# Performance work log

Hardware: AMD Instinct MI355X
Metric: run time of the kernel (lower is better)

The kernel has to match this reference:

```python
import jax, jax.numpy as jnp
import numpy as np

DIM = 256
HEADS = 4
HEAD_DIM = 32
HIDDEN = HEADS * HEAD_DIM  # 128
EPS = 1e-12  # F.normalize eps


def rmsnorm(x, g):
    # F.normalize(x, dim=1) * g * sqrt(C)
    n = jnp.sqrt(jnp.sum(x * x, axis=1, keepdims=True))
    return x / jnp.maximum(n, EPS) * g * jnp.sqrt(jnp.float32(x.shape[1]))


def setup_inputs() -> dict:
    key = jax.random.key(0)
    k1, k2, k3 = jax.random.split(key, 3)
    b, h, w = 16, 64, 64
    x = jax.random.normal(k1, (b, DIM, h, w), dtype=jnp.float32)
    # conv weights: kaiming-ish scale for 1x1 convs
    w_qkv = jax.random.normal(k2, (3 * HIDDEN, DIM), dtype=jnp.float32) / np.sqrt(DIM)
    w_out = jax.random.normal(k3, (DIM, HIDDEN), dtype=jnp.float32) / np.sqrt(HIDDEN)
    return {
        "x": x,
        "g_norm": jnp.ones((1, DIM, 1, 1), jnp.float32),
        "w_qkv": w_qkv,
        "w_out": w_out,
        "b_out": jnp.zeros((DIM,), jnp.float32),
        "g_out": jnp.ones((1, DIM, 1, 1), jnp.float32),
    }


def reference(x, g_norm, w_qkv, w_out, b_out, g_out):
    b, c, h, w = x.shape
    n = h * w
    scale = HEAD_DIM ** (-0.5)

    xn = rmsnorm(x, g_norm)
    # 1x1 conv == channel matmul: (3*hidden, c) x (b, c, h, w)
    qkv = jnp.einsum('oc,bchw->bohw', w_qkv, xn)
    qkv = qkv.reshape(b, 3, HEADS, HEAD_DIM, n)
    q, k, v = qkv[:, 0], qkv[:, 1], qkv[:, 2]  # each (b, heads, head_dim, n)

    q = jax.nn.softmax(q, axis=-2)  # over head_dim
    k = jax.nn.softmax(k, axis=-1)  # over spatial tokens

    # context = k @ v^T : (b, heads, d, d)
    context = jnp.einsum('bhdn,bhen->bhde', k, v)
    # out = context^T @ (q*scale) : (b, heads, d, n)
    out = jnp.einsum('bhde,bhdn->bhen', context, q * scale)
    out = out.reshape(b, HIDDEN, h, w)

    out = jnp.einsum('oc,bchw->bohw', w_out, out) + b_out[None, :, None, None]
    out = rmsnorm(out, g_out)
    return out
```

## Files before the change

### kernel.cpp

```cpp
#include <hip/hip_runtime.h>
#include <hip/hip_bf16.h>
#include <math.h>

#define B 16
#define C 256
#define H 4
#define D 32
#define HID 128
#define O3 384
#define N 4096
#define NSPLIT 32
#define QSCALE 0.17677669529663687f
#define RMS_MUL 16.0f
#define EPS 1e-12f

typedef __attribute__((ext_vector_type(8))) short short8;
typedef __attribute__((ext_vector_type(4))) float f32x4;

__device__ __forceinline__ ushort f2bf(float f) {
  __hip_bfloat16 h = __float2bfloat16(f);
  return *(ushort*)&h;
}
__device__ __forceinline__ float bf2f(ushort u) {
  unsigned int v = ((unsigned int)u) << 16;
  return *(float*)&v;
}
__device__ __forceinline__ void load_lds16(const void* g, void* l) {
  __builtin_amdgcn_global_load_lds((const __attribute__((address_space(1))) void*)g,
                                   (__attribute__((address_space(3))) void*)l, 16, 0, 0);
}

__global__ __launch_bounds__(256) void k_prep(const float* __restrict__ wqkv,
                                              const float* __restrict__ g,
                                              const float* __restrict__ x,
                                              ushort* __restrict__ wA,
                                              ushort* __restrict__ xbf) {
  __shared__ float red[8][32];
  __shared__ float invs[32];
  int t = threadIdx.x;
  if (blockIdx.x < 384) {
    int idx = blockIdx.x * 256 + t;
    wA[idx] = f2bf(wqkv[idx] * g[idx & (C - 1)]);
    return;
  }
  int id = blockIdx.x - 384;
  int g8 = t >> 5, ln = t & 31;
  int b = id >> 7, n0 = (id & 127) * 32;
  const float* xb = x + (size_t)b * C * N + n0 + ln;
  float v[32];
  float ss = 0.f;
  #pragma unroll
  for (int i = 0; i < 32; ++i) {
    v[i] = xb[(size_t)(g8 * 32 + i) * N];
    ss += v[i] * v[i];
  }
  red[g8][ln] = ss;
  __syncthreads();
  if (t < 32) {
    float tot = 0.f;
    #pragma unroll
    for (int j = 0; j < 8; ++j) tot += red[j][t];
    invs[t] = RMS_MUL / fmaxf(sqrtf(tot), EPS);
  }
  __syncthreads();
  float inv = invs[ln];
  ushort* dst = xbf + ((size_t)(b * N + n0 + ln)) * C + g8 * 32;
  #pragma unroll
  for (int ch = 0; ch < 4; ++ch) {
    union { ushort s[8]; uint4 q; } u;
    #pragma unroll
    for (int j = 0; j < 8; ++j) u.s[j] = f2bf(v[ch * 8 + j] * inv);
    *(uint4*)(dst + ch * 8) = u.q;
  }
}

__global__ __launch_bounds__(256, 4) void k_kvctx(const ushort* __restrict__ A,
                                                  const ushort* __restrict__ Bm,
                                                  float* __restrict__ ctxp) {
  const int K = 256;
  __shared__ ushort lds[16384];
  ushort* Abuf = lds;
  ushort* Bbuf = lds + 8192;
  int bid = blockIdx.x;
  int work = (bid & 7) * 128 + (bid >> 3);
  int mh = work & 1, sl = (work >> 1) & 31, b = work >> 6;
  int t = threadIdx.x;
  int lane = t & 63, w = t >> 6;
  int n0 = sl * 128;
  const ushort* Bb = Bm + ((size_t)b * N + n0) * K;
  f32x4 acc[2][8] = {};
  for (int k0 = 0; k0 < K; k0 += 64) {
    #pragma unroll
    for (int i = 0; i < 4; ++i) {
      int c = w * 4 + i;
      int lr = c * 8 + (lane >> 3);
      int gr = mh * 64 + (lr & 63) + ((lr & 64) << 1);
      int col = k0 + (lane & 7) * 8;
      load_lds16(A + (size_t)gr * K + col, Abuf + c * 512);
    }
    #pragma unroll
    for (int i = 0; i < 4; ++i) {
      int c = w * 4 + i;
      int row = c * 8 + (lane >> 3);
      int col = k0 + (lane & 7) * 8;
      load_lds16(Bb + (size_t)row * K + col, Bbuf + c * 512);
    }
    __syncthreads();
    #pragma unroll
    for (int kk = 0; kk < 2; ++kk) {
      short8 af[2], bfr[8];
      #pragma unroll
      for (int m = 0; m < 2; ++m)
        af[m] = *(const short8*)&Abuf[(w * 32 + m * 16 + (lane & 15)) * 64 + kk * 32 + (lane >> 4) * 8];
      #pragma unroll
      for (int nn = 0; nn < 8; ++nn)
        bfr[nn] = *(const short8*)&Bbuf[(nn * 16 + (lane & 15)) * 64 + kk * 32 + (lane >> 4) * 8];
      #pragma unroll
      for (int m = 0; m < 2; ++m)
        #pragma unroll
        for (int nn = 0; nn < 8; ++nn)
          acc[m][nn] = __builtin_amdgcn_mfma_f32_16x16x32_bf16(af[m], bfr[nn], acc[m][nn], 0, 0, 0);
    }
    __syncthreads();
  }
  float* cbb = ctxp + (size_t)(sl * 64 + b * 4) * 1056;
  if (w < 2) {
    #pragma unroll
    for (int m = 0; m < 2; ++m)
      #pragma unroll
      for (int nn = 0; nn < 8; ++nn)
        #pragma unroll
        for (int j = 0; j < 4; ++j) acc[m][nn][j] = __expf(acc[m][nn][j]);
    #pragma unroll
    for (int m = 0; m < 2; ++m)
      #pragma unroll
      for (int j = 0; j < 4; ++j) {
        float s = 0.f;
        #pragma unroll
        for (int nn = 0; nn < 8; ++nn) s += acc[m][nn][j];
        s += __shfl_xor(s, 1); s += __shfl_xor(s, 2);
        s += __shfl_xor(s, 4); s += __shfl_xor(s, 8);
        if ((lane & 15) == 0) {
          int lr = w * 32 + m * 16 + (lane >> 4) * 4 + j;
          int h = mh * 2 + (lr >> 5);
          cbb[(size_t)h * 1056 + 1024 + (lr & 31)] = s;
        }
      }
  }
  #pragma unroll
  for (int m = 0; m < 2; ++m)
    #pragma unroll
    for (int nn = 0; nn < 8; ++nn) {
      int lr0 = w * 32 + m * 16 + (lane >> 4) * 4;
      int n = nn * 16 + (lane & 15);
      #pragma unroll
      for (int j = 0; j < 4; ++j) {
        int lr = lr0 + j;
        lds[(lr * 128 + n) ^ ((lr & 7) << 3)] = f2bf(acc[m][nn][j]);
      }
    }
  __syncthreads();
  int hl = w >> 1, eh = w & 1;
  f32x4 cacc[2] = {};
  #pragma unroll
  for (int kk = 0; kk < 4; ++kk) {
    short8 af2[2], bv;
    #pragma unroll
    for (int m = 0; m < 2; ++m) {
      int lrk = hl * 32 + m * 16 + (lane & 15);
      af2[m] = *(const short8*)&lds[(lrk * 128 + kk * 32 + (lane >> 4) * 8) ^ ((lrk & 7) << 3)];
    }
    int lrv = 64 + hl * 32 + eh * 16 + (lane & 15);
    bv = *(const short8*)&lds[(lrv * 128 + kk * 32 + (lane >> 4) * 8) ^ ((lrv & 7) << 3)];
    #pragma unroll
    for (int m = 0; m < 2; ++m)
      cacc[m] = __builtin_amdgcn_mfma_f32_16x16x32_bf16(af2[m], bv, cacc[m], 0, 0, 0);
  }
  int hg = mh * 2 + hl;
  float* cb = ctxp + (size_t)(sl * 64 + b * 4 + hg) * 1056;
  #pragma unroll
  for (int m = 0; m < 2; ++m)
    #pragma unroll
    for (int j = 0; j < 4; ++j) {
      int d = m * 16 + (lane >> 4) * 4 + j;
      int e = eh * 16 + (lane & 15);
      cb[d * 32 + e] = cacc[m][j];
    }
}

__global__ __launch_bounds__(256) void k_redweff(const float* __restrict__ ctxp,
                                                 const float* __restrict__ wout,
                                                 ushort* __restrict__ Weff) {
  __shared__ float ctxn[D][D + 1];
  __shared__ float ksum[D];
  int bh = blockIdx.x;
  int b = bh >> 2, h = bh & 3;
  int t = threadIdx.x;
  int d = t >> 3, e0 = (t & 7) * 4;
  float vs[4] = {0.f, 0.f, 0.f, 0.f};
  float ks = 0.f;
  for (int s = 0; s < NSPLIT; ++s) {
    const float* cb = ctxp + (size_t)(s * 64 + bh) * 1056;
    f32x4 v = *(const f32x4*)(cb + d * 32 + e0);
    vs[0] += v[0]; vs[1] += v[1]; vs[2] += v[2]; vs[3] += v[3];
    if (t < 32) ks += cb[1024 + t];
  }
  if (t < 32) ksum[t] = ks;
  __syncthreads();
  float rk = 1.f / ksum[d];
  #pragma unroll
  for (int j = 0; j < 4; ++j) ctxn[d][e0 + j] = vs[j] * rk;
  __syncthreads();
  float wrow[D];
  #pragma unroll
  for (int e = 0; e < D; ++e) wrow[e] = wout[t * HID + h * D + e];
  ushort* wb = Weff + ((size_t)(b * C + t)) * HID + h * D;
  #pragma unroll
  for (int g = 0; g < 4; ++g) {
    union { ushort s[8]; uint4 v; } u;
    #pragma unroll
    for (int dj = 0; dj < 8; ++dj) {
      int dd = g * 8 + dj;
      float a = 0.f;
      #pragma unroll
      for (int e = 0; e < D; ++e) a += wrow[e] * ctxn[dd][e];
      u.s[dj] = f2bf(a);
    }
    *(uint4*)(wb + g * 8) = u.v;
  }
}

__global__ __launch_bounds__(256, 4) void k_qout(const ushort* __restrict__ A,
                                                 const ushort* __restrict__ Bm,
                                                 const ushort* __restrict__ WeffG,
                                                 const float* __restrict__ bias,
                                                 const float* __restrict__ g,
                                                 float* __restrict__ outp) {
  const int K = 256;
  __shared__ ushort lds[16384];
  ushort* Abuf = lds;
  ushort* Bbuf = lds + 8192;
  ushort* qlds = lds + 8192;
  ushort* A2buf = lds;
  int bid = blockIdx.x;
  int work = (bid & 7) * 128 + (bid >> 3);
  int xt = work & 63, b = work >> 6;
  int t = threadIdx.x;
  int lane = t & 63, w = t >> 6;
  int n0 = xt * 64;
  const ushort* Bb = Bm + ((size_t)b * N + n0) * K;
  {
    f32x4 acc[2][4] = {};
    for (int k0 = 0; k0 < K; k0 += 64) {
      #pragma unroll
      for (int i = 0; i < 4; ++i) {
        int c = w * 4 + i;
        int row = c * 8 + (lane >> 3);
        int col = k0 + (lane & 7) * 8;
        load_lds16(A + (size_t)row * K + col, Abuf + c * 512);
      }
      #pragma unroll
      for (int i = 0; i < 2; ++i) {
        int c = w * 2 + i;
        int row = c * 8 + (lane >> 3);
        int col = k0 + (lane & 7) * 8;
        load_lds16(Bb + (size_t)row * K + col, Bbuf + c * 512);
      }
      __syncthreads();
      #pragma unroll
      for (int kk = 0; kk < 2; ++kk) {
        short8 af[2], bfr[4];
        #pragma unroll
        for (int m = 0; m < 2; ++m)
          af[m] = *(const short8*)&Abuf[(w * 32 + m * 16 + (lane & 15)) * 64 + kk * 32 + (lane >> 4) * 8];
        #pragma unroll
        for (int nn = 0; nn < 4; ++nn)
          bfr[nn] = *(const short8*)&Bbuf[(nn * 16 + (lane & 15)) * 64 + kk * 32 + (lane >> 4) * 8];
        #pragma unroll
        for (int m = 0; m < 2; ++m)
          #pragma unroll
          for (int nn = 0; nn < 4; ++nn)
            acc[m][nn] = __builtin_amdgcn_mfma_f32_16x16x32_bf16(af[m], bfr[nn], acc[m][nn], 0, 0, 0);
      }
      __syncthreads();
    }
    #pragma unroll
    for (int nn = 0; nn < 4; ++nn) {
      float pm = -1e30f;
      #pragma unroll
      for (int m = 0; m < 2; ++m)
        #pragma unroll
        for (int j = 0; j < 4; ++j) pm = fmaxf(pm, acc[m][nn][j]);
      pm = fmaxf(pm, __shfl_xor(pm, 16));
      pm = fmaxf(pm, __shfl_xor(pm, 32));
      float e[2][4], ps = 0.f;
      #pragma unroll
      for (int m = 0; m < 2; ++m)
        #pragma unroll
        for (int j = 0; j < 4; ++j) {
          e[m][j] = __expf(acc[m][nn][j] - pm);
          ps += e[m][j];
        }
      ps += __shfl_xor(ps, 16);
      ps += __shfl_xor(ps, 32);
      float rs = QSCALE / ps;
      #pragma unroll
      for (int m = 0; m < 2; ++m)
        #pragma unroll
        for (int j = 0; j < 4; ++j) acc[m][nn][j] = e[m][j] * rs;
    }
    #pragma unroll
    for (int m = 0; m < 2; ++m)
      #pragma unroll
      for (int nn = 0; nn < 4; ++nn) {
        int d0 = w * 32 + m * 16 + (lane >> 4) * 4;
        int n = nn * 16 + (lane & 15);
        union { ushort us[4]; uint2 v; } u;
        #pragma unroll
        for (int j = 0; j < 4; ++j) u.us[j] = f2bf(acc[m][nn][j]);
        *(uint2*)&qlds[(n * 128 + d0) ^ ((n & 7) << 3)] = u.v;
      }
  }
  __syncthreads();
  const ushort* Aw = WeffG + (size_t)b * C * HID;
  f32x4 acc2[4][4] = {};
  for (int k0 = 0; k0 < HID; k0 += 32) {
    #pragma unroll
    for (int i = 0; i < 4; ++i) {
      int c = w * 4 + i;
      int row = c * 16 + (lane >> 2);
      int col = k0 + (lane & 3) * 8;
      load_lds16(Aw + (size_t)row * HID + col, A2buf + c * 512);
    }
    __syncthreads();
    short8 af[4], bfr[4];
    #pragma unroll
    for (int m = 0; m < 4; ++m)
      af[m] = *(const short8*)&A2buf[(w * 64 + m * 16 + (lane & 15)) * 32 + (lane >> 4) * 8];
    #pragma unroll
    for (int nn = 0; nn < 4; ++nn) {
      int n = nn * 16 + (lane & 15);
      bfr[nn] = *(const short8*)&qlds[(n * 128 + k0 + (lane >> 4) * 8) ^ ((n & 7) << 3)];
    }
    #pragma unroll
    for (int m = 0; m < 4; ++m)
      #pragma unroll
      for (int nn = 0; nn < 4; ++nn)
        acc2[m][nn] = __builtin_amdgcn_mfma_f32_16x16x32_bf16(af[m], bfr[nn], acc2[m][nn], 0, 0, 0);
    __syncthreads();
  }
  float* ssred = (float*)lds;
  #pragma unroll
  for (int m = 0; m < 4; ++m)
    #pragma unroll
    for (int j = 0; j < 4; ++j) {
      int row = w * 64 + m * 16 + (lane >> 4) * 4 + j;
      float bv = bias[row];
      #pragma unroll
      for (int nn = 0; nn < 4; ++nn) acc2[m][nn][j] += bv;
    }
  float ssp[4];
  #pragma unroll
  for (int nn = 0; nn < 4; ++nn) {
    float s = 0.f;
    #pragma unroll
    for (int m = 0; m < 4; ++m)
      #pragma unroll
      for (int j = 0; j < 4; ++j) s += acc2[m][nn][j] * acc2[m][nn][j];
    s += __shfl_xor(s, 16);
    s += __shfl_xor(s, 32);
    ssp[nn] = s;
  }
  if ((lane >> 4) == 0) {
    #pragma unroll
    for (int nn = 0; nn < 4; ++nn) ssred[w * 64 + nn * 16 + (lane & 15)] = ssp[nn];
  }
  __syncthreads();
  float inv[4];
  #pragma unroll
  for (int nn = 0; nn < 4; ++nn) {
    int col = nn * 16 + (lane & 15);
    float tot = ssred[col] + ssred[64 + col] + ssred[128 + col] + ssred[192 + col];
    inv[nn] = RMS_MUL / fmaxf(sqrtf(tot), EPS);
  }
  float* Cb = outp + (size_t)b * C * N + n0;
  #pragma unroll
  for (int m = 0; m < 4; ++m)
    #pragma unroll
    for (int j = 0; j < 4; ++j) {
      int row = w * 64 + m * 16 + (lane >> 4) * 4 + j;
      float gm = g[row];
      #pragma unroll
      for (int nn = 0; nn < 4; ++nn) {
        int col = nn * 16 + (lane & 15);
        Cb[(size_t)row * N + col] = acc2[m][nn][j] * inv[nn] * gm;
      }
    }
}

extern "C" void kernel_launch(void* const* d_in, const int* in_sizes, int n_in,
                              void* d_out, int out_size, void* d_ws, size_t ws_size,
                              hipStream_t stream) {
  const float* x    = (const float*)d_in[0];
  const float* gn   = (const float*)d_in[1];
  const float* wqkv = (const float*)d_in[2];
  const float* wout = (const float*)d_in[3];
  const float* bout = (const float*)d_in[4];
  const float* gout = (const float*)d_in[5];
  float* out = (float*)d_out;
  float* ws  = (float*)d_ws;

  ushort* xbf  = (ushort*)ws;
  float*  ctxp = ws + 8388608;
  ushort* Weff = (ushort*)(ws + 10551296);
  ushort* wA   = (ushort*)(ws + 10813440);

  k_prep   <<<2432, 256, 0, stream>>>(wqkv, gn, x, wA, xbf);
  k_kvctx  <<<1024, 256, 0, stream>>>(wA + 128 * 256, xbf, ctxp);
  k_redweff<<<64, 256, 0, stream>>>(ctxp, wout, Weff);
  k_qout   <<<1024, 256, 0, stream>>>(wA, xbf, Weff, bout, gout, out);
}
```

Baseline: 86.30 us.

## Double-buffer LDS staging in kvctx and qout GEMM loops

Restructures the K-loops of the two projection GEMM kernels into a two-stage ping-pong pipeline over K=32 slices. The next slice is issued via global_load_lds before computing the current one, with one waitcnt+barrier per iteration instead of two syncthreads. This is meant to hide global load latency behind MFMA work. The cost is smaller K per stage, which means more barriers overall, plus a hand-written waitcnt barrier that depends on correct ordering.

New measurement: 85.09 us. No clear change (-1.4%).

```diff
diff --git a/kernel.cpp b/kernel.cpp
--- a/kernel.cpp
+++ b/kernel.cpp
@@ -17,13 +17,11 @@
 typedef __attribute__((ext_vector_type(8))) short short8;
 typedef __attribute__((ext_vector_type(4))) float f32x4;
 
+#define VM0_BARRIER() asm volatile("s_waitcnt vmcnt(0)\ns_barrier" ::: "memory")
+
 __device__ __forceinline__ ushort f2bf(float f) {
   __hip_bfloat16 h = __float2bfloat16(f);
   return *(ushort*)&h;
-}
-__device__ __forceinline__ float bf2f(ushort u) {
-  unsigned int v = ((unsigned int)u) << 16;
-  return *(float*)&v;
 }
 __device__ __forceinline__ void load_lds16(const void* g, void* l) {
   __builtin_amdgcn_global_load_lds((const __attribute__((address_space(1))) void*)g,
@@ -79,8 +77,6 @@
                                                   float* __restrict__ ctxp) {
   const int K = 256;
   __shared__ ushort lds[16384];
-  ushort* Abuf = lds;
-  ushort* Bbuf = lds + 8192;
   int bid = blockIdx.x;
   int work = (bid & 7) * 128 + (bid >> 3);
   int mh = work & 1, sl = (work >> 1) & 31, b = work >> 6;
@@ -89,40 +85,48 @@
   int n0 = sl * 128;
   const ushort* Bb = Bm + ((size_t)b * N + n0) * K;
   f32x4 acc[2][8] = {};
-  for (int k0 = 0; k0 < K; k0 += 64) {
-    #pragma unroll
-    for (int i = 0; i < 4; ++i) {
-      int c = w * 4 + i;
-      int lr = c * 8 + (lane >> 3);
+
+  auto stage = [&](int buf, int k0) {
+    #pragma unroll
+    for (int i = 0; i < 2; ++i) {
+      int c = w * 2 + i;
+      int lr = c * 16 + (lane >> 2);
       int gr = mh * 64 + (lr & 63) + ((lr & 64) << 1);
-      int col = k0 + (lane & 7) * 8;
-      load_lds16(A + (size_t)gr * K + col, Abuf + c * 512);
-    }
-    #pragma unroll
-    for (int i = 0; i < 4; ++i) {
-      int c = w * 4 + i;
-      int row = c * 8 + (lane >> 3);
-      int col = k0 + (lane & 7) * 8;
-      load_lds16(Bb + (size_t)row * K + col, Bbuf + c * 512);
-    }
-    __syncthreads();
-    #pragma unroll
-    for (int kk = 0; kk < 2; ++kk) {
-      short8 af[2], bfr[8];
-      #pragma unroll
-      for (int m = 0; m < 2; ++m)
-        af[m] = *(const short8*)&Abuf[(w * 32 + m * 16 + (lane & 15)) * 64 + kk * 32 + (lane >> 4) * 8];
+      int col = k0 + (lane & 3) * 8;
+      load_lds16(A + (size_t)gr * K + col, lds + buf * 4096 + c * 512);
+    }
+    #pragma unroll
+    for (int i = 0; i < 2; ++i) {
+      int c = w * 2 + i;
+      int row = c * 16 + (lane >> 2);
+      int col = k0 + (lane & 3) * 8;
+      load_lds16(Bb + (size_t)row * K + col, lds + 8192 + buf * 4096 + c * 512);
+    }
+  };
+
+  stage(0, 0);
+  VM0_BARRIER();
+  #pragma unroll
+  for (int ki = 0; ki < 8; ++ki) {
+    int cur = ki & 1;
+    if (ki < 7) stage(cur ^ 1, (ki + 1) * 32);
+    const ushort* Ar = lds + cur * 4096;
+    const ushort* Br = lds + 8192 + cur * 4096;
+    short8 af[2], bfr[8];
+    #pragma unroll
+    for (int m = 0; m < 2; ++m)
+      af[m] = *(const short8*)&Ar[(w * 32 + m * 16 + (lane & 15)) * 32 + (lane >> 4) * 8];
+    #pragma unroll
+    for (int nn = 0; nn < 8; ++nn)
+      bfr[nn] = *(const short8*)&Br[(nn * 16 + (lane & 15)) * 32 + (lane >> 4) * 8];
+    #pragma unroll
+    for (int m = 0; m < 2; ++m)
       #pragma unroll
       for (int nn = 0; nn < 8; ++nn)
-        bfr[nn] = *(const short8*)&Bbuf[(nn * 16 + (lane & 15)) * 64 + kk * 32 + (lane >> 4) * 8];
-      #pragma unroll
-      for (int m = 0; m < 2; ++m)
-        #pragma unroll
-        for (int nn = 0; nn < 8; ++nn)
-          acc[m][nn] = __builtin_amdgcn_mfma_f32_16x16x32_bf16(af[m], bfr[nn], acc[m][nn], 0, 0, 0);
-    }
-    __syncthreads();
-  }
+        acc[m][nn] = __builtin_amdgcn_mfma_f32_16x16x32_bf16(af[m], bfr[nn], acc[m][nn], 0, 0, 0);
+    VM0_BARRIER();
+  }
+
   float* cbb = ctxp + (size_t)(sl * 64 + b * 4) * 1056;
   if (w < 2) {
     #pragma unroll
@@ -238,10 +242,7 @@
                                                  float* __restrict__ outp) {
   const int K = 256;
   __shared__ ushort lds[16384];
-  ushort* Abuf = lds;
-  ushort* Bbuf = lds + 8192;
   ushort* qlds = lds + 8192;
-  ushort* A2buf = lds;
   int bid = blockIdx.x;
   int work = (bid & 7) * 128 + (bid >> 3);
   int xt = work & 63, b = work >> 6;
@@ -250,39 +251,43 @@
   int n0 = xt * 64;
   const ushort* Bb = Bm + ((size_t)b * N + n0) * K;
   {
-    f32x4 acc[2][4] = {};
-    for (int k0 = 0; k0 < K; k0 += 64) {
-      #pragma unroll
-      for (int i = 0; i < 4; ++i) {
-        int c = w * 4 + i;
-        int row = c * 8 + (lane >> 3);
-        int col = k0 + (lane & 7) * 8;
-        load_lds16(A + (size_t)row * K + col, Abuf + c * 512);
-      }
+    auto stage1 = [&](int buf, int k0) {
       #pragma unroll
       for (int i = 0; i < 2; ++i) {
         int c = w * 2 + i;
-        int row = c * 8 + (lane >> 3);
-        int col = k0 + (lane & 7) * 8;
-        load_lds16(Bb + (size_t)row * K + col, Bbuf + c * 512);
-      }
-      __syncthreads();
-      #pragma unroll
-      for (int kk = 0; kk < 2; ++kk) {
-        short8 af[2], bfr[4];
-        #pragma unroll
-        for (int m = 0; m < 2; ++m)
-          af[m] = *(const short8*)&Abuf[(w * 32 + m * 16 + (lane & 15)) * 64 + kk * 32 + (lane >> 4) * 8];
+        int row = c * 16 + (lane >> 2);
+        int col = k0 + (lane & 3) * 8;
+        load_lds16(A + (size_t)row * K + col, lds + buf * 4096 + c * 512);
+      }
+      {
+        int c = w;
+        int row = c * 16 + (lane >> 2);
+        int col = k0 + (lane & 3) * 8;
+        load_lds16(Bb + (size_t)row * K + col, lds + 8192 + buf * 2048 + c * 512);
+      }
+    };
+    f32x4 acc[2][4] = {};
+    stage1(0, 0);
+    VM0_BARRIER();
+    #pragma unroll
+    for (int ki = 0; ki < 8; ++ki) {
+      int cur = ki & 1;
+      if (ki < 7) stage1(cur ^ 1, (ki + 1) * 32);
+      const ushort* Ar = lds + cur * 4096;
+      const ushort* Br = lds + 8192 + cur * 2048;
+      short8 af[2], bfr[4];
+      #pragma unroll
+      for (int m = 0; m < 2; ++m)
+        af[m] = *(const short8*)&Ar[(w * 32 + m * 16 + (lane & 15)) * 32 + (lane >> 4) * 8];
+      #pragma unroll
+      for (int nn = 0; nn < 4; ++nn)
+        bfr[nn] = *(const short8*)&Br[(nn * 16 + (lane & 15)) * 32 + (lane >> 4) * 8];
+      #pragma unroll
+      for (int m = 0; m < 2; ++m)
         #pragma unroll
         for (int nn = 0; nn < 4; ++nn)
-          bfr[nn] = *(const short8*)&Bbuf[(nn * 16 + (lane & 15)) * 64 + kk * 32 + (lane >> 4) * 8];
-        #pragma unroll
-        for (int m = 0; m < 2; ++m)
-          #pragma unroll
-          for (int nn = 0; nn < 4; ++nn)
-            acc[m][nn] = __builtin_amdgcn_mfma_f32_16x16x32_bf16(af[m], bfr[nn], acc[m][nn], 0, 0, 0);
-      }
-      __syncthreads();
+          acc[m][nn] = __builtin_amdgcn_mfma_f32_16x16x32_bf16(af[m], bfr[nn], acc[m][nn], 0, 0, 0);
+      VM0_BARRIER();
     }
     #pragma unroll
     for (int nn = 0; nn < 4; ++nn) {
@@ -323,6 +328,7 @@
   }
   __syncthreads();
   const ushort* Aw = WeffG + (size_t)b * C * HID;
+  ushort* A2buf = lds;
   f32x4 acc2[4][4] = {};
   for (int k0 = 0; k0 < HID; k0 += 32) {
     #pragma unroll
```
